# Kernel optimization log

Measured on AMD Instinct MI355X. Metric: run time of the kernel, lower is better.

The kernel has to match this reference:

```python
import jax, jax.numpy as jnp
import numpy as np

T, B, V, E, H, L = 128, 32, 50000, 512, 512, 2


def _lstm_layer(x, h0, c0, Wih, Whh, bih, bhh):
    # x: [T, B, in]; torch gate order i, f, g, o
    def step(carry, xt):
        h, c = carry
        gates = xt @ Wih.T + bih + h @ Whh.T + bhh  # [B, 4H]
        i, f, g, o = jnp.split(gates, 4, axis=-1)
        c = jax.nn.sigmoid(f) * c + jax.nn.sigmoid(i) * jnp.tanh(g)
        h = jax.nn.sigmoid(o) * jnp.tanh(c)
        return (h, c), h
    (h, c), ys = jax.lax.scan(step, (h0, c0), x)
    return ys, h, c


def setup_inputs() -> dict:
    key = jax.random.key(0)
    ks = jax.random.split(key, 12)
    s = 0.02
    return {
        'word': jax.random.randint(ks[0], (B,), 0, V),
        'seq': jax.random.randint(ks[1], (T, B), 0, V),
        'emb': jax.random.normal(ks[2], (V, E), jnp.float32) * s,
        'w2h_W': jax.random.normal(ks[3], (H, E), jnp.float32) * s,
        'w2h_b': jnp.zeros((H,), jnp.float32),
        'Wih0': jax.random.normal(ks[4], (4 * H, E), jnp.float32) * s,
        'Whh0': jax.random.normal(ks[5], (4 * H, H), jnp.float32) * s,
        'bih0': jnp.zeros((4 * H,), jnp.float32),
        'bhh0': jnp.zeros((4 * H,), jnp.float32),
        'Wih1': jax.random.normal(ks[6], (4 * H, H), jnp.float32) * s,
        'Whh1': jax.random.normal(ks[7], (4 * H, H), jnp.float32) * s,
        'bih1': jnp.zeros((4 * H,), jnp.float32),
        'bhh1': jnp.zeros((4 * H,), jnp.float32),
        'dec_W': jax.random.normal(ks[8], (V, H), jnp.float32) * s,
        'dec_b': jnp.zeros((V,), jnp.float32),
    }


def reference(word, seq, emb, w2h_W, w2h_b, Wih0, Whh0, bih0, bhh0,
              Wih1, Whh1, bih1, bhh1, dec_W, dec_b):
    word_emb = emb[word]                       # [B, E]
    seq_emb = emb[seq]                         # [T, B, E] (dropouts are 0/eval)
    # init_hidden: c0 = word2hidden(word_emb) expanded to all layers, h0 = 0
    c0 = word_emb @ w2h_W.T + w2h_b            # [B, H]
    h0 = jnp.zeros_like(c0)
    # 2-layer LSTM; stepping all layers per timestep == running layers sequentially
    y0, h_f0, c_f0 = _lstm_layer(seq_emb, h0, c0, Wih0, Whh0, bih0, bhh0)
    y1, h_f1, c_f1 = _lstm_layer(y0, h0, c0, Wih1, Whh1, bih1, bhh1)
    out = y1.reshape(T * B, H)                 # [T*B, H]
    decoded = out @ dec_W.T + dec_b            # [T*B, V]
    h_final = jnp.stack([h_f0, h_f1], axis=0)  # [L, B, H]
    c_final = jnp.stack([c_f0, c_f1], axis=0)
    return decoded, h_final, c_final
```

## Files before the change

kernel.cpp:

```cpp
#include <hip/hip_runtime.h>
#include <hip/hip_bf16.h>
#include <cstdint>

#define T_STEPS 128
#define BATCH   32
#define VOCAB   50000
#define EDIM    512
#define HDIM    512
#define GDIM    2048
#define MROWS   4096
#define VPAD    50048
#define BH      (BATCH * HDIM)

typedef short bf16x8 __attribute__((ext_vector_type(8)));
typedef float f32x4  __attribute__((ext_vector_type(4)));
typedef unsigned short us4 __attribute__((ext_vector_type(4)));
typedef unsigned short us8 __attribute__((ext_vector_type(8)));

#define MFMA16(a, b, c) __builtin_amdgcn_mfma_f32_16x16x32_bf16(a, b, c, 0, 0, 0)

__device__ __forceinline__ float fsigmoid(float x) {
    return 1.0f / (1.0f + __expf(-x));
}
__device__ __forceinline__ float ftanh(float x) {
    return 1.0f - 2.0f / (1.0f + __expf(2.0f * x));
}

__device__ __forceinline__ unsigned short f2bf(float f) {
    unsigned int u = __float_as_uint(f);
    u = (u + 0x7fffu + ((u >> 16) & 1u)) >> 16;
    return (unsigned short)u;
}


__global__ __launch_bounds__(256) void conv_decw(const float* __restrict__ src,
                                                 unsigned short* __restrict__ dst) {
    long i = ((long)blockIdx.x * 256 + threadIdx.x) * 8;
    if (i >= (long)VPAD * EDIM) return;
    long row = i >> 9;
    us8 v;
    if (row < VOCAB) {
        float4 a = *(const float4*)(src + i);
        float4 b = *(const float4*)(src + i + 4);
        v[0] = f2bf(a.x); v[1] = f2bf(a.y); v[2] = f2bf(a.z); v[3] = f2bf(a.w);
        v[4] = f2bf(b.x); v[5] = f2bf(b.y); v[6] = f2bf(b.z); v[7] = f2bf(b.w);
    } else {
        v = (us8)0;
    }
    *(us8*)(dst + i) = v;
}

__global__ __launch_bounds__(64) void pack_conv(const float* __restrict__ src,
                                                unsigned short* __restrict__ dst) {
    const int n = blockIdx.x;
    const int orig = (n & 3) * 512 + (n >> 2);
    const int k = threadIdx.x * 8;
    const float* s = src + (long)orig * 512 + k;
    float4 a = *(const float4*)s;
    float4 b = *(const float4*)(s + 4);
    us8 v;
    v[0] = f2bf(a.x); v[1] = f2bf(a.y); v[2] = f2bf(a.z); v[3] = f2bf(a.w);
    v[4] = f2bf(b.x); v[5] = f2bf(b.y); v[6] = f2bf(b.z); v[7] = f2bf(b.w);
    *(us8*)(dst + (long)n * 512 + k) = v;
}

__global__ __launch_bounds__(256) void pack_bias(const float* __restrict__ bih0,
                                                 const float* __restrict__ bhh0,
                                                 const float* __restrict__ bih1,
                                                 const float* __restrict__ bhh1,
                                                 float* __restrict__ b0p,
                                                 float* __restrict__ b1p) {
    const int n = blockIdx.x * 256 + threadIdx.x;
    const int orig = (n & 3) * 512 + (n >> 2);
    b0p[n] = bih0[orig] + bhh0[orig];
    b1p[n] = bih1[orig] + bhh1[orig];
}

__global__ __launch_bounds__(256) void gather_x(const int* __restrict__ seq,
                                                const float* __restrict__ emb,
                                                unsigned short* __restrict__ Xbf) {
    long i = ((long)blockIdx.x * 256 + threadIdx.x) * 4;
    if (i >= (long)MROWS * EDIM) return;
    int r   = (int)(i >> 9);
    int col = (int)(i & 511);
    const float* er = emb + (long)seq[r] * EDIM + col;
    float4 e = *(const float4*)er;
    us4 v;
    v[0] = f2bf(e.x); v[1] = f2bf(e.y); v[2] = f2bf(e.z); v[3] = f2bf(e.w);
    *(us4*)(Xbf + i) = v;
}

__global__ __launch_bounds__(256) void init_c0(const int* __restrict__ word,
                                               const float* __restrict__ emb,
                                               const float* __restrict__ w2hW,
                                               const float* __restrict__ w2hb,
                                               float* __restrict__ c0s, float* __restrict__ c1s,
                                               unsigned short* __restrict__ y0bf,
                                               unsigned short* __restrict__ y1bf) {
    const int idx = blockIdx.x * 256 + threadIdx.x;
    const int b = idx >> 9, hh = idx & 511;
    const float* er = emb + (long)word[b] * EDIM;
    const float* wr = w2hW + (long)hh * EDIM;
    float acc = w2hb[hh];
    #pragma unroll 4
    for (int k = 0; k < EDIM; k += 4) {
        float4 e4 = *(const float4*)(er + k);
        float4 w4 = *(const float4*)(wr + k);
        acc += e4.x * w4.x + e4.y * w4.y + e4.z * w4.z + e4.w * w4.w;
    }
    c0s[idx] = acc;
    c1s[idx] = acc;
    y0bf[idx] = 0;
    y1bf[idx] = 0;
}

__global__ __launch_bounds__(256) void gemm_bt128(const unsigned short* __restrict__ A,
                                                  const unsigned short* __restrict__ Bt,
                                                  float* __restrict__ C,
                                                  const float* __restrict__ bias1,
                                                  const float* __restrict__ bias2,
                                                  int K, int Nreal, long ldc, int ntn) {
    __shared__ __align__(16) unsigned char smem[34048];
    unsigned short* As = (unsigned short*)smem;
    unsigned short* Bs = (unsigned short*)(smem + 16384);
    float* ctile = (float*)smem;

    const int tid  = threadIdx.x;
    const long m0  = (long)(blockIdx.x / ntn) * 128;
    const long n0  = (long)(blockIdx.x % ntn) * 128;
    const int lane = tid & 63;
    const int wave = tid >> 6;
    const int wr = wave >> 1, wc = wave & 1;
    const int fr = lane & 15, fq = lane >> 4;

    f32x4 acc[4][4];
    #pragma unroll
    for (int i = 0; i < 4; ++i)
        #pragma unroll
        for (int j = 0; j < 4; ++j) acc[i][j] = (f32x4)0.0f;

    const int srow = tid >> 3;
    const int scol = (tid & 7) * 8;

    for (int kt = 0; kt < K; kt += 64) {
        #pragma unroll
        for (int i = 0; i < 4; ++i) {
            const unsigned short* ga = A  + (m0 + i * 32 + srow) * K + kt + scol;
            const unsigned short* gb = Bt + (n0 + i * 32 + srow) * K + kt + scol;
            __builtin_amdgcn_global_load_lds((const __attribute__((address_space(1))) void*)ga,
                                             (__attribute__((address_space(3))) void*)(As + i * 2048 + tid * 8),
                                             16, 0, 0);
            __builtin_amdgcn_global_load_lds((const __attribute__((address_space(1))) void*)gb,
                                             (__attribute__((address_space(3))) void*)(Bs + i * 2048 + tid * 8),
                                             16, 0, 0);
        }
        asm volatile("s_waitcnt vmcnt(0)" ::: "memory");
        __syncthreads();
        #pragma unroll
        for (int ks = 0; ks < 64; ks += 32) {
            bf16x8 af[4], bfr[4];
            #pragma unroll
            for (int mi = 0; mi < 4; ++mi)
                af[mi] = *(const bf16x8*)&As[(wr * 64 + mi * 16 + fr) * 64 + ks + fq * 8];
            #pragma unroll
            for (int ni = 0; ni < 4; ++ni)
                bfr[ni] = *(const bf16x8*)&Bs[(wc * 64 + ni * 16 + fr) * 64 + ks + fq * 8];
            #pragma unroll
            for (int mi = 0; mi < 4; ++mi)
                #pragma unroll
                for (int ni = 0; ni < 4; ++ni)
                    acc[mi][ni] = MFMA16(af[mi], bfr[ni], acc[mi][ni]);
        }
        __syncthreads();
    }

    #pragma unroll
    for (int h = 0; h < 2; ++h) {
        if (wr == h) {
            #pragma unroll
            for (int ni = 0; ni < 4; ++ni) {
                const long col = n0 + wc * 64 + ni * 16 + fr;
                float bs = 0.0f;
                if (col < Nreal)
                    bs = (bias1 ? bias1[col] : 0.0f) + (bias2 ? bias2[col] : 0.0f);
                #pragma unroll
                for (int mi = 0; mi < 4; ++mi)
                    #pragma unroll
                    for (int r = 0; r < 4; ++r)
                        ctile[(mi * 16 + fq * 4 + r) * 132 + wc * 64 + ni * 16 + fr] =
                            acc[mi][ni][r] + bs;
            }
        }
        __syncthreads();
        #pragma unroll
        for (int j = 0; j < 8; ++j) {
            const int flat = tid + j * 256;
            const int row = flat >> 5, colq = flat & 31;
            const long col4 = n0 + colq * 4;
            if (col4 < Nreal) {
                f32x4 v = *(const f32x4*)&ctile[row * 132 + colq * 4];
                *(f32x4*)&C[(m0 + h * 64 + row) * ldc + col4] = v;
            }
        }
        __syncthreads();
    }
}

__global__ __launch_bounds__(512) void lstm_step2(
        const float* __restrict__ G0,
        const unsigned short* __restrict__ Whh0p,
        const unsigned short* __restrict__ Wih1p,
        const unsigned short* __restrict__ Whh1p,
        const float* __restrict__ b1p,
        unsigned short* __restrict__ y0bf,
        unsigned short* __restrict__ y1bf,
        float* __restrict__ c0s, float* __restrict__ c1s,
        float* __restrict__ hf,
        int t) {
    __shared__ float part[8][32][32];
    int bid = blockIdx.x;
    const int tid  = threadIdx.x;
    const int wv   = tid >> 6, lane = tid & 63;
    const int fr   = lane & 15, fq = lane >> 4;

    int layer, tt, cg;
    if (bid < 64) { layer = 0; tt = t;     if (tt >= T_STEPS) return; cg = bid; }
    else          { layer = 1; tt = t - 1; if (tt < 0) return;       cg = bid - 64; }

    const unsigned short* hin;
    unsigned short* yout;
    float* cs;
    if (layer == 0) { hin = y0bf + (long)tt * BH; yout = y0bf + (long)(tt + 1) * BH; cs = c0s; }
    else            { hin = y1bf + (long)tt * BH; yout = y1bf + (long)(tt + 1) * BH; cs = c1s; }

    const int n_base = cg * 32;

    const int pb = tid >> 3, pu = tid & 7;
    const int si = pb * HDIM + cg * 8 + pu;
    float creg = 0.0f;
    float4 ad = make_float4(0.f, 0.f, 0.f, 0.f);
    if (tid < 256) {
        creg = cs[si];
        if (layer == 0) ad = *(const float4*)(G0 + ((long)tt * BATCH + pb) * GDIM + n_base + pu * 4);
        else            ad = *(const float4*)(b1p + n_base + pu * 4);
    }

    f32x4 acc[2][2];
    acc[0][0] = (f32x4)0.0f; acc[0][1] = (f32x4)0.0f;
    acc[1][0] = (f32x4)0.0f; acc[1][1] = (f32x4)0.0f;

    if (layer == 0) {
        const int kbase = wv * 64;
        const unsigned short* A0 = hin + fr * 512 + kbase + fq * 8;
        const unsigned short* A1 = A0 + 16 * 512;
        const unsigned short* B0 = Whh0p + (long)(n_base + fr) * 512 + kbase + fq * 8;
        const unsigned short* B1 = B0 + 16 * 512;
        #pragma unroll
        for (int i = 0; i < 2; ++i) {
            bf16x8 a0 = *(const bf16x8*)(A0 + i * 32);
            bf16x8 a1 = *(const bf16x8*)(A1 + i * 32);
            bf16x8 b0 = *(const bf16x8*)(B0 + i * 32);
            bf16x8 b1 = *(const bf16x8*)(B1 + i * 32);
            acc[0][0] = MFMA16(a0, b0, acc[0][0]);
            acc[0][1] = MFMA16(a0, b1, acc[0][1]);
            acc[1][0] = MFMA16(a1, b0, acc[1][0]);
            acc[1][1] = MFMA16(a1, b1, acc[1][1]);
        }
    } else {
        const unsigned short* Aop = (wv < 4) ? (y0bf + (long)(tt + 1) * BH) : hin;
        const unsigned short* Bop = (wv < 4) ? Wih1p : Whh1p;
        const int kbase = (wv & 3) * 128;
        const unsigned short* A0 = Aop + fr * 512 + kbase + fq * 8;
        const unsigned short* A1 = A0 + 16 * 512;
        const unsigned short* B0 = Bop + (long)(n_base + fr) * 512 + kbase + fq * 8;
        const unsigned short* B1 = B0 + 16 * 512;
        #pragma unroll
        for (int i = 0; i < 4; ++i) {
            bf16x8 a0 = *(const bf16x8*)(A0 + i * 32);
            bf16x8 a1 = *(const bf16x8*)(A1 + i * 32);
            bf16x8 b0 = *(const bf16x8*)(B0 + i * 32);
            bf16x8 b1 = *(const bf16x8*)(B1 + i * 32);
            acc[0][0] = MFMA16(a0, b0, acc[0][0]);
            acc[0][1] = MFMA16(a0, b1, acc[0][1]);
            acc[1][0] = MFMA16(a1, b0, acc[1][0]);
            acc[1][1] = MFMA16(a1, b1, acc[1][1]);
        }
    }

    #pragma unroll
    for (int mi = 0; mi < 2; ++mi)
        #pragma unroll
        for (int ni = 0; ni < 2; ++ni)
            #pragma unroll
            for (int r = 0; r < 4; ++r)
                part[wv][mi * 16 + fq * 4 + r][ni * 16 + fr] = acc[mi][ni][r];
    __syncthreads();

    if (tid < 256) {
        float4 g4 = *(const float4*)&part[0][pb][pu * 4];
        #pragma unroll
        for (int w = 1; w < 8; ++w) {
            float4 p4 = *(const float4*)&part[w][pb][pu * 4];
            g4.x += p4.x; g4.y += p4.y; g4.z += p4.z; g4.w += p4.w;
        }
        const float vi = g4.x + ad.x, vf = g4.y + ad.y;
        const float vg = g4.z + ad.z, vo = g4.w + ad.w;
        float c = fsigmoid(vf) * creg + fsigmoid(vi) * ftanh(vg);
        float h = fsigmoid(vo) * ftanh(c);
        cs[si] = c;
        yout[si] = f2bf(h);
        if (tt == T_STEPS - 1) hf[layer * BH + si] = h;
    }
}

__global__ __launch_bounds__(256) void finalize_states(const float* __restrict__ hf,
                                                       const float* __restrict__ c0s,
                                                       const float* __restrict__ c1s,
                                                       float* __restrict__ out) {
    const int idx = blockIdx.x * 256 + threadIdx.x;
    const long base = (long)MROWS * VOCAB;
    float v;
    if (idx < 32768)      v = hf[idx];
    else if (idx < 49152) v = c0s[idx - 32768];
    else                  v = c1s[idx - 49152];
    out[base + idx] = v;
}

extern "C" void kernel_launch(void* const* d_in, const int* in_sizes, int n_in,
                              void* d_out, int out_size, void* d_ws, size_t ws_size,
                              hipStream_t stream) {
    const int*   word  = (const int*)d_in[0];
    const int*   seq   = (const int*)d_in[1];
    const float* emb   = (const float*)d_in[2];
    const float* w2hW  = (const float*)d_in[3];
    const float* w2hb  = (const float*)d_in[4];
    const float* Wih0  = (const float*)d_in[5];
    const float* Whh0  = (const float*)d_in[6];
    const float* bih0  = (const float*)d_in[7];
    const float* bhh0  = (const float*)d_in[8];
    const float* Wih1  = (const float*)d_in[9];
    const float* Whh1  = (const float*)d_in[10];
    const float* bih1  = (const float*)d_in[11];
    const float* bhh1  = (const float*)d_in[12];
    const float* dec_W = (const float*)d_in[13];
    const float* dec_b = (const float*)d_in[14];
    float* out = (float*)d_out;

    char* ws = (char*)d_ws;
    size_t off = 0;
    float*          G0    = (float*)(ws + off);          off += (size_t)MROWS * GDIM * 4;
    unsigned short* Xbf   = (unsigned short*)(ws + off); off += (size_t)MROWS * EDIM * 2;
    unsigned short* Wih0p = (unsigned short*)(ws + off); off += (size_t)GDIM  * EDIM * 2;
    unsigned short* Whh0p = (unsigned short*)(ws + off); off += (size_t)GDIM  * HDIM * 2;
    unsigned short* Wih1p = (unsigned short*)(ws + off); off += (size_t)GDIM  * HDIM * 2;
    unsigned short* Whh1p = (unsigned short*)(ws + off); off += (size_t)GDIM  * HDIM * 2;
    unsigned short* decWb = (unsigned short*)(ws + off); off += (size_t)VPAD  * EDIM * 2;
    unsigned short* y0bf  = (unsigned short*)(ws + off); off += (size_t)(T_STEPS + 1) * BH * 2;
    unsigned short* y1bf  = (unsigned short*)(ws + off); off += (size_t)(T_STEPS + 1) * BH * 2;
    float* b0p = (float*)(ws + off); off += (size_t)GDIM * 4;
    float* b1p = (float*)(ws + off); off += (size_t)GDIM * 4;
    float* c0s = (float*)(ws + off); off += (size_t)BH * 4;
    float* c1s = (float*)(ws + off); off += (size_t)BH * 4;
    float* hf  = (float*)(ws + off); off += (size_t)2 * BH * 4;

    conv_decw<<<12512, 256, 0, stream>>>(dec_W, decWb);
    pack_conv<<<2048, 64, 0, stream>>>(Wih0, Wih0p);
    pack_conv<<<2048, 64, 0, stream>>>(Whh0, Whh0p);
    pack_conv<<<2048, 64, 0, stream>>>(Wih1, Wih1p);
    pack_conv<<<2048, 64, 0, stream>>>(Whh1, Whh1p);
    pack_bias<<<8, 256, 0, stream>>>(bih0, bhh0, bih1, bhh1, b0p, b1p);
    gather_x<<<2048, 256, 0, stream>>>(seq, emb, Xbf);
    init_c0<<<64, 256, 0, stream>>>(word, emb, w2hW, w2hb, c0s, c1s, y0bf, y1bf);

    gemm_bt128<<<32 * 16, 256, 0, stream>>>(Xbf, Wih0p, G0, b0p, nullptr,
                                            512, GDIM, (long)GDIM, 16);

    for (int t = 0; t <= T_STEPS; ++t)
        lstm_step2<<<128, 512, 0, stream>>>(G0, Whh0p, Wih1p, Whh1p, b1p,
                                            y0bf, y1bf, c0s, c1s, hf, t);

    gemm_bt128<<<32 * 391, 256, 0, stream>>>(y1bf + BH, decWb, out, dec_b, nullptr,
                                             512, VOCAB, (long)VOCAB, 391);

    finalize_states<<<256, 256, 0, stream>>>(hf, c0s, c1s, out);
}
```

Before: 1.359 ms.

## Overlap decoder weight conversion with LSTM steps and band decoder GEMM tiles

Converting the decoder weight matrix to bf16 no longer runs as a separate kernel. The work is split across 224 extra blocks added to each of the 129 recurrent step launches, so it runs on compute units the latency-bound step kernel leaves idle. The four LSTM weight packing launches are merged into one kernel. The decoder GEMM now walks tiles in bands of 23 column tiles across all row tiles, so the weight tiles are reused from L2. The risk is that the extra conversion blocks compete with the recurrent blocks for memory bandwidth and scheduling on the critical path.

Result: no change. 1.375 ms (+1.1%).

```diff
diff --git a/kernel.cpp b/kernel.cpp
--- a/kernel.cpp
+++ b/kernel.cpp
@@ -11,6 +11,7 @@
 #define MROWS   4096
 #define VPAD    50048
 #define BH      (BATCH * HDIM)
+#define CONV_BLOCKS 224
 
 typedef short bf16x8 __attribute__((ext_vector_type(8)));
 typedef float f32x4  __attribute__((ext_vector_type(4)));
@@ -33,26 +34,18 @@
 }
 
 
-__global__ __launch_bounds__(256) void conv_decw(const float* __restrict__ src,
-                                                 unsigned short* __restrict__ dst) {
-    long i = ((long)blockIdx.x * 256 + threadIdx.x) * 8;
-    if (i >= (long)VPAD * EDIM) return;
-    long row = i >> 9;
-    us8 v;
-    if (row < VOCAB) {
-        float4 a = *(const float4*)(src + i);
-        float4 b = *(const float4*)(src + i + 4);
-        v[0] = f2bf(a.x); v[1] = f2bf(a.y); v[2] = f2bf(a.z); v[3] = f2bf(a.w);
-        v[4] = f2bf(b.x); v[5] = f2bf(b.y); v[6] = f2bf(b.z); v[7] = f2bf(b.w);
-    } else {
-        v = (us8)0;
-    }
-    *(us8*)(dst + i) = v;
-}
-
-__global__ __launch_bounds__(64) void pack_conv(const float* __restrict__ src,
-                                                unsigned short* __restrict__ dst) {
-    const int n = blockIdx.x;
+__global__ __launch_bounds__(64) void pack_all(const float* __restrict__ s0,
+                                               const float* __restrict__ s1,
+                                               const float* __restrict__ s2,
+                                               const float* __restrict__ s3,
+                                               unsigned short* __restrict__ d0,
+                                               unsigned short* __restrict__ d1,
+                                               unsigned short* __restrict__ d2,
+                                               unsigned short* __restrict__ d3) {
+    const int which = blockIdx.x >> 11;
+    const int n = blockIdx.x & 2047;
+    const float* src = (which == 0) ? s0 : (which == 1) ? s1 : (which == 2) ? s2 : s3;
+    unsigned short* dst = (which == 0) ? d0 : (which == 1) ? d1 : (which == 2) ? d2 : d3;
     const int orig = (n & 3) * 512 + (n >> 2);
     const int k = threadIdx.x * 8;
     const float* s = src + (long)orig * 512 + k;
@@ -119,15 +112,24 @@
                                                   float* __restrict__ C,
                                                   const float* __restrict__ bias1,
                                                   const float* __restrict__ bias2,
-                                                  int K, int Nreal, long ldc, int ntn) {
+                                                  int K, int Nreal, long ldc, int ntn,
+                                                  int banded) {
     __shared__ __align__(16) unsigned char smem[34048];
     unsigned short* As = (unsigned short*)smem;
     unsigned short* Bs = (unsigned short*)(smem + 16384);
     float* ctile = (float*)smem;
 
     const int tid  = threadIdx.x;
-    const long m0  = (long)(blockIdx.x / ntn) * 128;
-    const long n0  = (long)(blockIdx.x % ntn) * 128;
+    long m0, n0;
+    if (banded) {
+        const int band  = blockIdx.x / 736;
+        const int local = blockIdx.x % 736;
+        m0 = (long)(local / 23) * 128;
+        n0 = (long)(band * 23 + local % 23) * 128;
+    } else {
+        m0 = (long)(blockIdx.x / ntn) * 128;
+        n0 = (long)(blockIdx.x % ntn) * 128;
+    }
     const int lane = tid & 63;
     const int wave = tid >> 6;
     const int wr = wave >> 1, wc = wave & 1;
@@ -216,10 +218,31 @@
         unsigned short* __restrict__ y1bf,
         float* __restrict__ c0s, float* __restrict__ c1s,
         float* __restrict__ hf,
+        const float* __restrict__ decW,
+        unsigned short* __restrict__ decWb,
         int t) {
     __shared__ float part[8][32][32];
     int bid = blockIdx.x;
     const int tid  = threadIdx.x;
+
+    if (bid >= 128) {
+        const long cid = (long)(bid - 128) + (long)t * CONV_BLOCKS;
+        const long i = (cid * 512 + tid) * 8;
+        if (i >= (long)VPAD * EDIM) return;
+        const long row = i >> 9;
+        us8 v;
+        if (row < VOCAB) {
+            float4 a = *(const float4*)(decW + i);
+            float4 b = *(const float4*)(decW + i + 4);
+            v[0] = f2bf(a.x); v[1] = f2bf(a.y); v[2] = f2bf(a.z); v[3] = f2bf(a.w);
+            v[4] = f2bf(b.x); v[5] = f2bf(b.y); v[6] = f2bf(b.z); v[7] = f2bf(b.w);
+        } else {
+            v = (us8)0;
+        }
+        *(us8*)(decWb + i) = v;
+        return;
+    }
+
     const int wv   = tid >> 6, lane = tid & 63;
     const int fr   = lane & 15, fq = lane >> 4;
 
@@ -363,24 +386,22 @@
     float* c1s = (float*)(ws + off); off += (size_t)BH * 4;
     float* hf  = (float*)(ws + off); off += (size_t)2 * BH * 4;
 
-    conv_decw<<<12512, 256, 0, stream>>>(dec_W, decWb);
-    pack_conv<<<2048, 64, 0, stream>>>(Wih0, Wih0p);
-    pack_conv<<<2048, 64, 0, stream>>>(Whh0, Whh0p);
-    pack_conv<<<2048, 64, 0, stream>>>(Wih1, Wih1p);
-    pack_conv<<<2048, 64, 0, stream>>>(Whh1, Whh1p);
+    pack_all<<<4 * 2048, 64, 0, stream>>>(Wih0, Whh0, Wih1, Whh1,
+                                          Wih0p, Whh0p, Wih1p, Whh1p);
     pack_bias<<<8, 256, 0, stream>>>(bih0, bhh0, bih1, bhh1, b0p, b1p);
     gather_x<<<2048, 256, 0, stream>>>(seq, emb, Xbf);
     init_c0<<<64, 256, 0, stream>>>(word, emb, w2hW, w2hb, c0s, c1s, y0bf, y1bf);
 
     gemm_bt128<<<32 * 16, 256, 0, stream>>>(Xbf, Wih0p, G0, b0p, nullptr,
-                                            512, GDIM, (long)GDIM, 16);
+                                            512, GDIM, (long)GDIM, 16, 0);
 
     for (int t = 0; t <= T_STEPS; ++t)
-        lstm_step2<<<128, 512, 0, stream>>>(G0, Whh0p, Wih1p, Whh1p, b1p,
-                                            y0bf, y1bf, c0s, c1s, hf, t);
+        lstm_step2<<<128 + CONV_BLOCKS, 512, 0, stream>>>(
+            G0, Whh0p, Wih1p, Whh1p, b1p, y0bf, y1bf, c0s, c1s, hf,
+            dec_W, decWb, t);
 
     gemm_bt128<<<32 * 391, 256, 0, stream>>>(y1bf + BH, decWb, out, dec_b, nullptr,
-                                             512, VOCAB, (long)VOCAB, 391);
+                                             512, VOCAB, (long)VOCAB, 391, 1);
 
     finalize_states<<<256, 256, 0, stream>>>(hf, c0s, c1s, out);
 }
```
